# Optimization experiments

Measured on AMD Instinct MI355X. Metric: run time of the kernel, lower is better.

## Reference

```python
import jax, jax.numpy as jnp
import numpy as np

STRIDE = 16.0
PRE = 1000      # rpn_pre_nms_top_n_test
POST = 500      # rpn_post_nms_top_n_test
NMS_TH = 0.7    # rpn_nms_thresh
POOL = 7        # roi align output_size
BBOX_CLIP = float(np.log(1000.0 / 16.0))


def make_anchors(H, W):
    sizes = jnp.array([32., 64., 128., 256.], jnp.float32)
    ratios = jnp.array([0.5, 1.0, 2.0], jnp.float32)
    hr = jnp.sqrt(ratios)
    wr = 1.0 / hr
    ws = (wr[:, None] * sizes[None, :]).reshape(-1)   # [12]
    hs = (hr[:, None] * sizes[None, :]).reshape(-1)
    base = jnp.stack([-ws / 2, -hs / 2, ws / 2, hs / 2], 1)  # [12,4]
    sy = jnp.arange(H, dtype=jnp.float32) * STRIDE
    sx = jnp.arange(W, dtype=jnp.float32) * STRIDE
    gy, gx = jnp.meshgrid(sy, sx, indexing='ij')
    shift = jnp.stack([gx, gy, gx, gy], -1)                  # [H,W,4]
    return (shift[:, :, None, :] + base[None, None]).reshape(-1, 4)  # [H*W*12,4]


def decode(anch, dlt):
    wa = anch[:, 2] - anch[:, 0]
    ha = anch[:, 3] - anch[:, 1]
    cxa = anch[:, 0] + 0.5 * wa
    cya = anch[:, 1] + 0.5 * ha
    dx, dy = dlt[:, 0], dlt[:, 1]
    dw = jnp.minimum(dlt[:, 2], BBOX_CLIP)
    dh = jnp.minimum(dlt[:, 3], BBOX_CLIP)
    cx = dx * wa + cxa
    cy = dy * ha + cya
    w = jnp.exp(dw) * wa
    h = jnp.exp(dh) * ha
    return jnp.stack([cx - 0.5 * w, cy - 0.5 * h, cx + 0.5 * w, cy + 0.5 * h], 1)


def box_iou(a, b):
    area_a = (a[:, 2] - a[:, 0]) * (a[:, 3] - a[:, 1])
    area_b = (b[:, 2] - b[:, 0]) * (b[:, 3] - b[:, 1])
    lt = jnp.maximum(a[:, None, :2], b[None, :, :2])
    rb = jnp.minimum(a[:, None, 2:], b[None, :, 2:])
    wh = jnp.clip(rb - lt, 0.0)
    inter = wh[..., 0] * wh[..., 1]
    return inter / (area_a[:, None] + area_b[None, :] - inter + 1e-6)


def bilinear(feat, ys, xs):
    # feat [C,H,W]; ys/xs [...]; returns [C, ...]
    H, W = feat.shape[1], feat.shape[2]
    ys = jnp.clip(ys, 0.0, H - 1.0)
    xs = jnp.clip(xs, 0.0, W - 1.0)
    y0 = jnp.floor(ys).astype(jnp.int32)
    x0 = jnp.floor(xs).astype(jnp.int32)
    y1 = jnp.minimum(y0 + 1, H - 1)
    x1 = jnp.minimum(x0 + 1, W - 1)
    wy = ys - y0
    wx = xs - x0
    return (feat[:, y0, x0] * (1 - wy) * (1 - wx)
            + feat[:, y0, x1] * (1 - wy) * wx
            + feat[:, y1, x0] * wy * (1 - wx)
            + feat[:, y1, x1] * wy * wx)


def roi_align(feat, boxes):
    # feat [C,H,W], boxes [N,4] in image coords; output_size=7, sampling_ratio=2
    N = boxes.shape[0]
    x1, y1 = boxes[:, 0] / STRIDE, boxes[:, 1] / STRIDE
    x2, y2 = boxes[:, 2] / STRIDE, boxes[:, 3] / STRIDE
    rw = jnp.maximum(x2 - x1, 1.0)
    rh = jnp.maximum(y2 - y1, 1.0)
    bw = rw / POOL
    bh = rh / POOL
    sub = (jnp.arange(2, dtype=jnp.float32) + 0.5) / 2.0  # 2 samples per bin dim
    grid = jnp.arange(POOL, dtype=jnp.float32)
    gy = y1[:, None, None] + (grid[None, :, None] + sub[None, None, :]) * bh[:, None, None]  # [N,7,2]
    gx = x1[:, None, None] + (grid[None, :, None] + sub[None, None, :]) * bw[:, None, None]
    ys = jnp.broadcast_to(gy[:, :, None, :, None], (N, POOL, POOL, 2, 2))
    xs = jnp.broadcast_to(gx[:, None, :, None, :], (N, POOL, POOL, 2, 2))
    v = bilinear(feat, ys, xs)          # [C,N,7,7,2,2]
    v = v.mean(axis=(-1, -2))           # avg over sample points -> [C,N,7,7]
    return v.transpose(1, 0, 2, 3).reshape(N, -1)  # [N, C*49]


def per_image(feat, obj, dlt, anchors, Himg, Wimg):
    sc, idx = jax.lax.top_k(obj, PRE)            # score-sorted (desc) pre-NMS proposals
    boxes = decode(anchors[idx], dlt[idx])
    boxes = jnp.stack([jnp.clip(boxes[:, 0], 0.0, Wimg), jnp.clip(boxes[:, 1], 0.0, Himg),
                       jnp.clip(boxes[:, 2], 0.0, Wimg), jnp.clip(boxes[:, 3], 0.0, Himg)], 1)
    iou = box_iou(boxes, boxes)                  # [PRE,PRE]
    ar = jnp.arange(PRE)

    def body(i, mask):
        cur = mask[i]
        sup = cur & (iou[i] > NMS_TH) & (ar > i)
        return mask & ~sup

    mask = jax.lax.fori_loop(0, PRE, body, jnp.ones((PRE,), bool))
    scm = jnp.where(mask, sc, -jnp.inf)
    _, keep = jax.lax.top_k(scm, POST)           # first POST kept (score order)
    props = boxes[keep]                          # [POST,4]
    return roi_align(feat, props)


def setup_inputs() -> dict:
    key = jax.random.key(0)
    ks = jax.random.split(key, 8)
    s = 0.02
    C, H, W = 960, 20, 40
    return {
        'features': jax.random.normal(ks[0], (2, C, H, W), jnp.float32),
        'rpn_conv_w': jax.random.normal(ks[1], (C, C, 3, 3), jnp.float32) * s,
        'rpn_conv_b': jnp.zeros((C,), jnp.float32),
        'rpn_cls_w': jax.random.normal(ks[2], (12, C), jnp.float32) * s,
        'rpn_cls_b': jnp.zeros((12,), jnp.float32),
        'rpn_reg_w': jax.random.normal(ks[3], (48, C), jnp.float32) * s,
        'rpn_reg_b': jnp.zeros((48,), jnp.float32),
        'fc6_w': jax.random.normal(ks[4], (C * POOL * POOL, 1024), jnp.float32) * s,
        'fc6_b': jnp.zeros((1024,), jnp.float32),
        'fc7_w': jax.random.normal(ks[5], (1024, 1024), jnp.float32) * s,
        'fc7_b': jnp.zeros((1024,), jnp.float32),
        'cls_w': jax.random.normal(ks[6], (1024, 5), jnp.float32) * s,
        'cls_b': jnp.zeros((5,), jnp.float32),
        'bbox_w': jax.random.normal(ks[7], (1024, 20), jnp.float32) * s,
        'bbox_b': jnp.zeros((20,), jnp.float32),
    }


def reference(features, rpn_conv_w, rpn_conv_b, rpn_cls_w, rpn_cls_b,
              rpn_reg_w, rpn_reg_b, fc6_w, fc6_b, fc7_w, fc7_b,
              cls_w, cls_b, bbox_w, bbox_b):
    B, C, H, W = features.shape
    A = 12
    t = jax.lax.conv_general_dilated(features, rpn_conv_w, (1, 1), 'SAME',
                                     dimension_numbers=('NCHW', 'OIHW', 'NCHW'))
    t = jax.nn.relu(t + rpn_conv_b[None, :, None, None])
    obj = (jnp.einsum('bchw,ac->bhwa', t, rpn_cls_w) + rpn_cls_b).reshape(B, -1)  # [B, H*W*A]
    reg = jnp.einsum('bchw,ac->bahw', t, rpn_reg_w) + rpn_reg_b[None, :, None, None]
    reg = reg.reshape(B, A, 4, H, W).transpose(0, 3, 4, 1, 2).reshape(B, -1, 4)   # [B, H*W*A, 4]
    anchors = make_anchors(H, W)
    Himg, Wimg = H * STRIDE, W * STRIDE
    pooled = jax.vmap(lambda f, o, d: per_image(f, o, d, anchors, Himg, Wimg))(
        features, obj, reg)                       # [B, POST, C*49]
    x = jax.nn.relu(pooled @ fc6_w + fc6_b)       # TwoMLPHead fc6
    x = jax.nn.relu(x @ fc7_w + fc7_b)            # TwoMLPHead fc7
    logits = x @ cls_w + cls_b                    # [B, POST, 5]
    breg = x @ bbox_w + bbox_b                    # [B, POST, 20]
    return jnp.concatenate([logits, breg], -1)    # [B, POST, 25]
```

## Files before the change

kernel.cpp:

```cpp
#include <hip/hip_runtime.h>
#include <hip/hip_bf16.h>
#include <cstdint>
#include <cstddef>


typedef __attribute__((ext_vector_type(8))) short short8;
typedef __attribute__((ext_vector_type(4))) float f32x4;

__device__ __forceinline__ void gld_lds16(const void* g, void* l)
{
  __builtin_amdgcn_global_load_lds(
      (const __attribute__((address_space(1))) unsigned int*)g,
      (__attribute__((address_space(3))) unsigned int*)l, 16, 0, 0);
}

__global__ __launch_bounds__(256) void pad_kernel(const float* __restrict__ f,
                                                  float* __restrict__ xp)
{
  int idx = blockIdx.x * 256 + threadIdx.x;
  const int total = 2 * 960 * 22 * 42;
  if (idx >= total) return;
  int xx = idx % 42;
  int r  = idx / 42;
  int yy = r % 22;
  int bc = r / 22;
  float v = 0.f;
  if (yy >= 1 && yy <= 20 && xx >= 1 && xx <= 40)
    v = f[bc * 800 + (yy - 1) * 40 + (xx - 1)];
  xp[idx] = v;
}

__global__ __launch_bounds__(256) void conv_kernel(const float* __restrict__ Wc,
                                                   const float* __restrict__ Xpad,
                                                   const float* __restrict__ bias,
                                                   float* __restrict__ T)
{
  __shared__ float As[16][64];
  __shared__ float Bs[16][64];
  int tid = threadIdx.x;
  int b  = blockIdx.z;
  int p0 = blockIdx.x * 64;
  int m0 = blockIdx.y * 64;
  int ty = tid >> 4, tx = tid & 15;
  int a_m = tid >> 2, a_k4 = (tid & 3) << 2;
  int b_k = tid >> 4, b_p4 = (tid & 15) << 2;
  const float* xb = Xpad + (size_t)b * 960 * 22 * 42;
  float acc[4][4] = {};
  for (int k0 = 0; k0 < 8640; k0 += 16) {
    float4 av = *(const float4*)&Wc[(size_t)(m0 + a_m) * 8640 + k0 + a_k4];
    As[a_k4 + 0][a_m] = av.x; As[a_k4 + 1][a_m] = av.y;
    As[a_k4 + 2][a_m] = av.z; As[a_k4 + 3][a_m] = av.w;
    int k = k0 + b_k;
    int c = k / 9; int tap = k - c * 9;
    int ky = tap / 3; int kx = tap - ky * 3;
    const float* xrow = xb + (c * 22 + ky) * 42 + kx;
#pragma unroll
    for (int u = 0; u < 4; ++u) {
      int p = p0 + b_p4 + u;
      float v = 0.f;
      if (p < 800) { int y = p / 40; int x = p - y * 40; v = xrow[y * 42 + x]; }
      Bs[b_k][b_p4 + u] = v;
    }
    __syncthreads();
#pragma unroll
    for (int kk = 0; kk < 16; ++kk) {
      float a[4], bb[4];
      *(float4*)a  = *(const float4*)&As[kk][ty << 2];
      *(float4*)bb = *(const float4*)&Bs[kk][tx << 2];
#pragma unroll
      for (int i = 0; i < 4; ++i)
#pragma unroll
        for (int j = 0; j < 4; ++j) acc[i][j] += a[i] * bb[j];
    }
    __syncthreads();
  }
#pragma unroll
  for (int i = 0; i < 4; ++i) {
    int o = m0 + (ty << 2) + i;
    float bs = bias[o];
#pragma unroll
    for (int j = 0; j < 4; ++j) {
      int p = p0 + (tx << 2) + j;
      if (p < 800) T[((size_t)b * 960 + o) * 800 + p] = fmaxf(acc[i][j] + bs, 0.f);
    }
  }
}

__global__ __launch_bounds__(256) void rpn_head(const float* __restrict__ t,
                                                const float* __restrict__ cls_w,
                                                const float* __restrict__ cls_b,
                                                const float* __restrict__ reg_w,
                                                const float* __restrict__ reg_b,
                                                float* __restrict__ obj,
                                                float* __restrict__ dlt)
{
  int bp = blockIdx.x;
  int b = bp / 800, p = bp - (bp / 800) * 800;
  __shared__ float tv[960];
  for (int c = threadIdx.x; c < 960; c += 256)
    tv[c] = t[((size_t)b * 960 + c) * 800 + p];
  __syncthreads();
  __shared__ float part[60][4];
  int j = threadIdx.x >> 2, pp = threadIdx.x & 3;
  if (j < 60) {
    const float* wrow = (j < 12) ? &cls_w[j * 960] : &reg_w[(j - 12) * 960];
    float acc = 0.f;
    for (int c = pp; c < 960; c += 4) acc += tv[c] * wrow[c];
    part[j][pp] = acc;
  }
  __syncthreads();
  if (threadIdx.x < 60) {
    int j2 = threadIdx.x;
    float s = part[j2][0] + part[j2][1] + part[j2][2] + part[j2][3];
    if (j2 < 12) {
      obj[(size_t)b * 9600 + p * 12 + j2] = s + cls_b[j2];
    } else {
      int o = j2 - 12;
      dlt[((size_t)b * 9600 + p * 12 + (o >> 2)) * 4 + (o & 3)] = s + reg_b[o];
    }
  }
}

__device__ inline unsigned long long pack_key(float v, int g)
{
  unsigned u = __float_as_uint(v);
  u = (u & 0x80000000u) ? ~u : (u | 0x80000000u);
  return ((unsigned long long)u << 32) | (unsigned)(~g);
}

__global__ __launch_bounds__(512) void sort8k(const float* __restrict__ obj,
                                              unsigned long long* __restrict__ topkeys)
{
  __shared__ unsigned long long keys[8192];
  int b = blockIdx.x >> 1, h = blockIdx.x & 1;
  int tid = threadIdx.x;
  for (int i = tid; i < 8192; i += 512) {
    int g = h * 8192 + i;
    unsigned long long key = 0ULL;
    if (g < 9600) key = pack_key(obj[(size_t)b * 9600 + g], g);
    keys[i] = key;
  }
  __syncthreads();
  for (int k = 2; k <= 8192; k <<= 1)
    for (int j = k >> 1; j > 0; j >>= 1) {
      for (int i = tid; i < 8192; i += 512) {
        int ixj = i ^ j;
        if (ixj > i) {
          bool desc = ((i & k) == 0);
          unsigned long long a = keys[i], c = keys[ixj];
          if ((a < c) == desc) { keys[i] = c; keys[ixj] = a; }
        }
      }
      __syncthreads();
    }
  for (int i = tid; i < 1024; i += 512)
    topkeys[(size_t)blockIdx.x * 1024 + i] = keys[i];
}

__global__ __launch_bounds__(256) void merge2k(const unsigned long long* __restrict__ topkeys,
                                               int* __restrict__ selidx)
{
  __shared__ unsigned long long keys[2048];
  int b = blockIdx.x, tid = threadIdx.x;
  for (int i = tid; i < 2048; i += 256) keys[i] = topkeys[(size_t)b * 2048 + i];
  __syncthreads();
  for (int k = 2; k <= 2048; k <<= 1)
    for (int j = k >> 1; j > 0; j >>= 1) {
      for (int i = tid; i < 2048; i += 256) {
        int ixj = i ^ j;
        if (ixj > i) {
          bool desc = ((i & k) == 0);
          unsigned long long a = keys[i], c = keys[ixj];
          if ((a < c) == desc) { keys[i] = c; keys[ixj] = a; }
        }
      }
      __syncthreads();
    }
  for (int i = tid; i < 1000; i += 256)
    selidx[b * 1000 + i] = (int)(~(unsigned)(keys[i] & 0xffffffffULL));
}

__global__ __launch_bounds__(256) void decode_kernel(const int* __restrict__ selidx,
                                                     const float* __restrict__ dlt,
                                                     float* __restrict__ boxes)
{
#pragma clang fp contract(off)
  int t = blockIdx.x * 256 + threadIdx.x;
  if (t >= 2000) return;
  int b = t / 1000;
  int g = selidx[t];
  int cell = g / 12, a = g - cell * 12;
  int y = cell / 40, x = cell - y * 40;
  int ridx = a >> 2, sidx = a & 3;
  const float sizes_[4]  = {32.f, 64.f, 128.f, 256.f};
  const float ratios_[3] = {0.5f, 1.f, 2.f};
  float size = sizes_[sidx];
  float hr = sqrtf(ratios_[ridx]);
  float wr = 1.f / hr;
  float wsz = wr * size, hsz = hr * size;
  float hw = 0.5f * wsz, hh = 0.5f * hsz;
  float gx = (float)x * 16.f, gy = (float)y * 16.f;
  float a0 = gx - hw, a1 = gy - hh, a2 = gx + hw, a3 = gy + hh;
  float wa = a2 - a0, ha = a3 - a1;
  float cxa = a0 + 0.5f * wa, cya = a1 + 0.5f * ha;
  const float* d = &dlt[(size_t)(b * 9600 + g) * 4];
  float dx = d[0], dy = d[1];
  float dw = fminf(d[2], 4.135166556742356f);
  float dh = fminf(d[3], 4.135166556742356f);
  float cx = dx * wa + cxa;
  float cy = dy * ha + cya;
  float w = expf(dw) * wa;
  float h = expf(dh) * ha;
  float x1 = cx - 0.5f * w, y1 = cy - 0.5f * h;
  float x2 = cx + 0.5f * w, y2 = cy + 0.5f * h;
  x1 = fminf(fmaxf(x1, 0.f), 640.f);
  y1 = fminf(fmaxf(y1, 0.f), 320.f);
  x2 = fminf(fmaxf(x2, 0.f), 640.f);
  y2 = fminf(fmaxf(y2, 0.f), 320.f);
  *(float4*)&boxes[(size_t)t * 4] = make_float4(x1, y1, x2, y2);
}

__global__ __launch_bounds__(256) void iou_kernel(const float* __restrict__ boxes,
                                                  unsigned long long* __restrict__ bitrow)
{
#pragma clang fp contract(off)
  int b = blockIdx.y;
  int i = blockIdx.x * 16 + (threadIdx.x >> 4);
  int w = threadIdx.x & 15;
  __shared__ float4 bx[1000];
  for (int t = threadIdx.x; t < 1000; t += 256)
    bx[t] = *(const float4*)&boxes[(size_t)(b * 1000 + t) * 4];
  __syncthreads();
  if (i >= 1000) return;
  float4 bi = bx[i];
  float area_i = (bi.z - bi.x) * (bi.w - bi.y);
  unsigned long long bits = 0ULL;
  for (int t = 0; t < 64; ++t) {
    int j = w * 64 + t;
    if (j > i && j < 1000) {
      float4 bj = bx[j];
      float xx1 = fmaxf(bi.x, bj.x), yy1 = fmaxf(bi.y, bj.y);
      float xx2 = fminf(bi.z, bj.z), yy2 = fminf(bi.w, bj.w);
      float iw = fmaxf(xx2 - xx1, 0.f), ih = fmaxf(yy2 - yy1, 0.f);
      float inter = iw * ih;
      float area_j = (bj.z - bj.x) * (bj.w - bj.y);
      float iou = inter / (area_i + area_j - inter + 1e-6f);
      if (iou > 0.7f) bits |= 1ULL << t;
    }
  }
  bitrow[(size_t)(b * 1000 + i) * 16 + w] = bits;
}

__device__ inline unsigned long long shfl64(unsigned long long v, int src)
{
  int lo = __shfl((int)(unsigned)(v & 0xffffffffULL), src, 64);
  int hi = __shfl((int)(unsigned)(v >> 32), src, 64);
  return ((unsigned long long)(unsigned)hi << 32) | (unsigned)lo;
}

__global__ __launch_bounds__(64) void nms_scan(const unsigned long long* __restrict__ bitrow,
                                               const float* __restrict__ boxes,
                                               float* __restrict__ props)
{
  int b = blockIdx.x;
  int lane = threadIdx.x;
  unsigned long long alive = 0ULL;
  if (lane < 15) alive = ~0ULL;
  else if (lane == 15) alive = (1ULL << 40) - 1ULL;
  const unsigned long long* rows = bitrow + (size_t)b * 16000;
  for (int i0 = 0; i0 < 1000; i0 += 4) {
    unsigned long long v = rows[i0 * 16 + lane];
#pragma unroll
    for (int s = 0; s < 4; ++s) {
      int i = i0 + s;
      unsigned long long row = shfl64(v, (s << 4) | (lane & 15));
      unsigned long long ow = shfl64(alive, i >> 6);
      if ((ow >> (i & 63)) & 1ULL) alive &= ~row;
    }
  }
  __shared__ unsigned long long am[16];
  __shared__ int keep[500];
  if (lane < 16) am[lane] = alive;
  __syncthreads();
  if (lane == 0) {
    int cnt = 0;
    for (int i = 0; i < 1000 && cnt < 500; ++i)
      if ((am[i >> 6] >> (i & 63)) & 1ULL) keep[cnt++] = i;
    for (int i = 0; i < 1000 && cnt < 500; ++i)
      if (!((am[i >> 6] >> (i & 63)) & 1ULL)) keep[cnt++] = i;
  }
  __syncthreads();
  for (int r = lane; r < 500; r += 64) {
    int g = keep[r];
    *(float4*)&props[(size_t)(b * 500 + r) * 4] =
        *(const float4*)&boxes[(size_t)(b * 1000 + g) * 4];
  }
}

__global__ __launch_bounds__(256) void transpose_feat(const float* __restrict__ f,
                                                      float* __restrict__ ft)
{
  __shared__ float tile[32][33];
  int b = blockIdx.z;
  int c0 = blockIdx.y * 32, p0 = blockIdx.x * 32;
  int tx = threadIdx.x, ty = threadIdx.y;
  for (int r = ty; r < 32; r += 8)
    tile[r][tx] = f[((size_t)b * 960 + c0 + r) * 800 + p0 + tx];
  __syncthreads();
  for (int r = ty; r < 32; r += 8)
    ft[((size_t)b * 800 + p0 + r) * 960 + c0 + tx] = tile[tx][r];
}

__global__ __launch_bounds__(256) void roi_kernel(const float* __restrict__ ft,
                                                  const float* __restrict__ props,
                                                  __hip_bfloat16* __restrict__ pooled)
{
  int q = blockIdx.x;
  int nr = blockIdx.y;
  __hip_bfloat16* outp = pooled + (size_t)nr * 47040 + q * 960;
  if (nr >= 1000) {
    for (int c = threadIdx.x; c < 960; c += 256) outp[c] = __float2bfloat16(0.f);
    return;
  }
  int b = nr / 500;
  int py = q / 7, px = q - py * 7;
  float4 bx = *(const float4*)&props[(size_t)nr * 4];
  float x1 = bx.x / 16.f, y1 = bx.y / 16.f, x2 = bx.z / 16.f, y2 = bx.w / 16.f;
  float rw = fmaxf(x2 - x1, 1.f), rh = fmaxf(y2 - y1, 1.f);
  float bw = rw / 7.f, bh = rh / 7.f;
  int offs[16]; float wts[16];
#pragma unroll
  for (int s = 0; s < 4; ++s) {
    int sy = s >> 1, sx = s & 1;
    float ys = y1 + ((float)py + (sy ? 0.75f : 0.25f)) * bh;
    float xs = x1 + ((float)px + (sx ? 0.75f : 0.25f)) * bw;
    ys = fminf(fmaxf(ys, 0.f), 19.f);
    xs = fminf(fmaxf(xs, 0.f), 39.f);
    int y0 = (int)floorf(ys), x0 = (int)floorf(xs);
    int y1i = y0 + 1 < 19 ? y0 + 1 : 19;
    int x1i = x0 + 1 < 39 ? x0 + 1 : 39;
    float wy = ys - (float)y0, wx = xs - (float)x0;
    int base0 = y0 * 40, base1 = y1i * 40;
    offs[s * 4 + 0] = base0 + x0;  wts[s * 4 + 0] = 0.25f * (1.f - wy) * (1.f - wx);
    offs[s * 4 + 1] = base0 + x1i; wts[s * 4 + 1] = 0.25f * (1.f - wy) * wx;
    offs[s * 4 + 2] = base1 + x0;  wts[s * 4 + 2] = 0.25f * wy * (1.f - wx);
    offs[s * 4 + 3] = base1 + x1i; wts[s * 4 + 3] = 0.25f * wy * wx;
  }
  const float* fb = ft + (size_t)b * 800 * 960;
  for (int c = threadIdx.x; c < 960; c += 256) {
    float acc = 0.f;
#pragma unroll
    for (int s = 0; s < 16; ++s) acc += wts[s] * fb[(size_t)offs[s] * 960 + c];
    outp[c] = __float2bfloat16(acc);
  }
}

__global__ __launch_bounds__(256) void cast_w6(const float* __restrict__ w6,
                                               __hip_bfloat16* __restrict__ WbT)
{
  __shared__ float tile[32][33];
  int c0 = blockIdx.x * 32;
  int n0 = blockIdx.y * 32;
  int q  = blockIdx.z;
  int tx = threadIdx.x & 31, ty = threadIdx.x >> 5;
  for (int rr = ty; rr < 32; rr += 8)
    tile[rr][tx] = w6[((size_t)(c0 + rr) * 49 + q) * 1024 + n0 + tx];
  __syncthreads();
  for (int rr = ty; rr < 32; rr += 8)
    WbT[(size_t)(n0 + rr) * 47040 + q * 960 + c0 + tx] = __float2bfloat16(tile[tx][rr]);
}

__global__ __launch_bounds__(256) void cast_w7(const float* __restrict__ w7,
                                               __hip_bfloat16* __restrict__ WT)
{
  __shared__ float tile[32][33];
  int k0 = blockIdx.x * 32, n0 = blockIdx.y * 32;
  int tx = threadIdx.x & 31, ty = threadIdx.x >> 5;
  for (int rr = ty; rr < 32; rr += 8)
    tile[rr][tx] = w7[(size_t)(k0 + rr) * 1024 + n0 + tx];
  __syncthreads();
  for (int rr = ty; rr < 32; rr += 8)
    WT[(size_t)(n0 + rr) * 1024 + k0 + tx] = __float2bfloat16(tile[tx][rr]);
}

__global__ __launch_bounds__(256, 2) void gemm_bf16(const ushort* __restrict__ A,
                                                    const ushort* __restrict__ BT,
                                                    float* __restrict__ C,
                                                    int Klen, int ksteps, int splitk)
{
  __shared__ __align__(16) ushort As[128 * 32];
  __shared__ __align__(16) ushort Bs[128 * 32];
  int tid = threadIdx.x;
  int wave = tid >> 6, lane = tid & 63;
  int n0 = blockIdx.x * 128, m0 = blockIdx.y * 128;
  int steps_per = (ksteps + splitk - 1) / splitk;
  int s0 = blockIdx.z * steps_per;
  int s1 = min(ksteps, s0 + steps_per);

  const ushort* Ap0 = A  + (size_t)(m0 + wave * 32 + (lane >> 2)) * Klen + ((lane & 3) << 3);
  const ushort* Bp0 = BT + (size_t)(n0 + wave * 32 + (lane >> 2)) * Klen + ((lane & 3) << 3);
  size_t rstep = (size_t)16 * Klen;
  ushort* Al0 = &As[(wave * 32) * 32];
  ushort* Al1 = &As[(wave * 32 + 16) * 32];
  ushort* Bl0 = &Bs[(wave * 32) * 32];
  ushort* Bl1 = &Bs[(wave * 32 + 16) * 32];

  int wm = (wave >> 1) * 64, wn = (wave & 1) * 64;
  int ar = lane & 15, aq = (lane >> 4) << 3;
  f32x4 acc[4][4] = {};

  for (int s = s0; s < s1; ++s) {
    size_t k0 = (size_t)s << 5;
    gld_lds16(Ap0 + k0, Al0);
    gld_lds16(Ap0 + rstep + k0, Al1);
    gld_lds16(Bp0 + k0, Bl0);
    gld_lds16(Bp0 + rstep + k0, Bl1);
    __syncthreads();
    short8 af[4], bfv[4];
#pragma unroll
    for (int mi = 0; mi < 4; ++mi)
      af[mi] = *(const short8*)&As[(wm + mi * 16 + ar) * 32 + aq];
#pragma unroll
    for (int ni = 0; ni < 4; ++ni)
      bfv[ni] = *(const short8*)&Bs[(wn + ni * 16 + ar) * 32 + aq];
#pragma unroll
    for (int mi = 0; mi < 4; ++mi)
#pragma unroll
      for (int ni = 0; ni < 4; ++ni)
        acc[mi][ni] = __builtin_amdgcn_mfma_f32_16x16x32_bf16(af[mi], bfv[ni],
                                                              acc[mi][ni], 0, 0, 0);
    __syncthreads();
  }
  int crow = m0 + wm + ((lane >> 4) << 2);
  int ccol = n0 + wn + (lane & 15);
#pragma unroll
  for (int mi = 0; mi < 4; ++mi)
#pragma unroll
    for (int ni = 0; ni < 4; ++ni) {
      float* cp = &C[(size_t)(crow + mi * 16) * 1024 + ccol + ni * 16];
      f32x4 v = acc[mi][ni];
      atomicAdd(cp,        v.x);
      atomicAdd(cp + 1024, v.y);
      atomicAdd(cp + 2048, v.z);
      atomicAdd(cp + 3072, v.w);
    }
}

__global__ __launch_bounds__(256) void ep_bf16(const float* __restrict__ Cacc,
                                               const float* __restrict__ bias,
                                               __hip_bfloat16* __restrict__ out)
{
  int idx = blockIdx.x * 256 + threadIdx.x;
  out[idx] = __float2bfloat16(fmaxf(Cacc[idx] + bias[idx & 1023], 0.f));
}

__global__ __launch_bounds__(256) void ep_f32(const float* __restrict__ Cacc,
                                              const float* __restrict__ bias,
                                              float* __restrict__ out)
{
  int idx = blockIdx.x * 256 + threadIdx.x;
  out[idx] = fmaxf(Cacc[idx] + bias[idx & 1023], 0.f);
}

__global__ __launch_bounds__(256) void out_head(const float* __restrict__ x2,
                                                const float* __restrict__ cls_w,
                                                const float* __restrict__ cls_b,
                                                const float* __restrict__ bbox_w,
                                                const float* __restrict__ bbox_b,
                                                float* __restrict__ out)
{
  int n = blockIdx.x;
  __shared__ float xv[1024];
  __shared__ float part[25][8];
  for (int k = threadIdx.x; k < 1024; k += 256) xv[k] = x2[(size_t)n * 1024 + k];
  __syncthreads();
  int j = threadIdx.x >> 3, pp = threadIdx.x & 7;
  if (j < 25) {
    float acc = 0.f;
    if (j < 5) {
      for (int k = pp; k < 1024; k += 8) acc += xv[k] * cls_w[k * 5 + j];
    } else {
      int jj = j - 5;
      for (int k = pp; k < 1024; k += 8) acc += xv[k] * bbox_w[k * 20 + jj];
    }
    part[j][pp] = acc;
  }
  __syncthreads();
  if (threadIdx.x < 25) {
    int j2 = threadIdx.x;
    float s = 0.f;
#pragma unroll
    for (int p = 0; p < 8; ++p) s += part[j2][p];
    s += (j2 < 5) ? cls_b[j2] : bbox_b[j2 - 5];
    out[(size_t)n * 25 + j2] = s;
  }
}

extern "C" void kernel_launch(void* const* d_in, const int* in_sizes, int n_in,
                              void* d_out, int out_size, void* d_ws, size_t ws_size,
                              hipStream_t stream)
{
  const float* features  = (const float*)d_in[0];
  const float* conv_w    = (const float*)d_in[1];
  const float* conv_b    = (const float*)d_in[2];
  const float* rpn_cls_w = (const float*)d_in[3];
  const float* rpn_cls_b = (const float*)d_in[4];
  const float* rpn_reg_w = (const float*)d_in[5];
  const float* rpn_reg_b = (const float*)d_in[6];
  const float* fc6_w     = (const float*)d_in[7];
  const float* fc6_b     = (const float*)d_in[8];
  const float* fc7_w     = (const float*)d_in[9];
  const float* fc7_b     = (const float*)d_in[10];
  const float* hd_cls_w  = (const float*)d_in[11];
  const float* hd_cls_b  = (const float*)d_in[12];
  const float* hd_bbox_w = (const float*)d_in[13];
  const float* hd_bbox_b = (const float*)d_in[14];

  char* ws = (char*)d_ws;
  size_t off = 0;
  auto alloc = [&](size_t bytes) -> char* {
    char* p = ws + off;
    off += (bytes + 255) & ~(size_t)255;
    return p;
  };
  float* xpad   = (float*)alloc(2ull * 960 * 22 * 42 * 4);
  float* t      = (float*)alloc(2ull * 960 * 800 * 4);
  float* obj    = (float*)alloc(2ull * 9600 * 4);
  float* dlt    = (float*)alloc(2ull * 9600 * 4 * 4);
  unsigned long long* topkeys = (unsigned long long*)alloc(4ull * 1024 * 8);
  int* selidx   = (int*)alloc(2000ull * 4);
  float* boxes  = (float*)alloc(2ull * 1000 * 4 * 4);
  unsigned long long* bitrow = (unsigned long long*)alloc(2ull * 1000 * 16 * 8);
  float* props  = (float*)alloc(2ull * 500 * 4 * 4);
  float* featT  = (float*)alloc(2ull * 800 * 960 * 4);
  __hip_bfloat16* pooled = (__hip_bfloat16*)alloc(1024ull * 47040 * 2);
  __hip_bfloat16* WbT    = (__hip_bfloat16*)alloc(1024ull * 47040 * 2);
  __hip_bfloat16* fc7T   = (__hip_bfloat16*)alloc(1024ull * 1024 * 2);
  float* Cacc   = (float*)alloc(1024ull * 1024 * 4);
  float* Cacc2  = (float*)alloc(1024ull * 1024 * 4);
  __hip_bfloat16* x1bf = (__hip_bfloat16*)alloc(1024ull * 1024 * 2);
  float* x2buf  = (float*)alloc(1024ull * 1024 * 4);

  hipMemsetAsync(Cacc, 0, 1024ull * 1024 * 4, stream);
  hipMemsetAsync(Cacc2, 0, 1024ull * 1024 * 4, stream);

  pad_kernel<<<(2 * 960 * 22 * 42 + 255) / 256, 256, 0, stream>>>(features, xpad);
  conv_kernel<<<dim3(13, 15, 2), 256, 0, stream>>>(conv_w, xpad, conv_b, t);
  rpn_head<<<1600, 256, 0, stream>>>(t, rpn_cls_w, rpn_cls_b, rpn_reg_w, rpn_reg_b, obj, dlt);
  sort8k<<<4, 512, 0, stream>>>(obj, topkeys);
  merge2k<<<2, 256, 0, stream>>>(topkeys, selidx);
  decode_kernel<<<8, 256, 0, stream>>>(selidx, dlt, boxes);
  iou_kernel<<<dim3(63, 2), 256, 0, stream>>>(boxes, bitrow);
  nms_scan<<<2, 64, 0, stream>>>(bitrow, boxes, props);
  transpose_feat<<<dim3(25, 30, 2), dim3(32, 8), 0, stream>>>(features, featT);
  roi_kernel<<<dim3(49, 1024), 256, 0, stream>>>(featT, props, pooled);
  cast_w6<<<dim3(30, 32, 49), 256, 0, stream>>>(fc6_w, WbT);
  cast_w7<<<dim3(32, 32), 256, 0, stream>>>(fc7_w, fc7T);
  gemm_bf16<<<dim3(8, 8, 8), 256, 0, stream>>>((const ushort*)pooled, (const ushort*)WbT,
                                               Cacc, 47040, 1470, 8);
  ep_bf16<<<4096, 256, 0, stream>>>(Cacc, fc6_b, x1bf);
  gemm_bf16<<<dim3(8, 8, 8), 256, 0, stream>>>((const ushort*)x1bf, (const ushort*)fc7T,
                                               Cacc2, 1024, 32, 8);
  ep_f32<<<4096, 256, 0, stream>>>(Cacc2, fc7_b, x2buf);
  out_head<<<1000, 256, 0, stream>>>(x2buf, hd_cls_w, hd_cls_b, hd_bbox_w, hd_bbox_b,
                                     (float*)d_out);
}
```

Baseline: 2.024 ms.

## Run RPN conv as split-bf16 MFMA GEMM and tile RPN head as GEMM

Replaces the FP32 SIMT 3x3 conv with an im2col GEMM on bf16 MFMA. Each FP32 operand is split into three bf16 parts, and six cross products are accumulated with atomics so precision stays near FP32. The per-pixel RPN head kernel becomes a tiled small GEMM over a padded activation layout. This costs extra preprocessing and memory traffic for the split weights and im2col buffers, plus atomic accumulation, and it reuses the workspace region of the pooled buffer.

```diff
diff --git a/kernel.cpp b/kernel.cpp
--- a/kernel.cpp
+++ b/kernel.cpp
@@ -7,6 +7,10 @@
 typedef __attribute__((ext_vector_type(8))) short short8;
 typedef __attribute__((ext_vector_type(4))) float f32x4;
 
+#define CONV_M 1024
+#define CONV_N 896
+#define CONV_K 8640
+
 __device__ __forceinline__ void gld_lds16(const void* g, void* l)
 {
   __builtin_amdgcn_global_load_lds(
@@ -14,79 +18,165 @@
       (__attribute__((address_space(3))) unsigned int*)l, 16, 0, 0);
 }
 
-__global__ __launch_bounds__(256) void pad_kernel(const float* __restrict__ f,
-                                                  float* __restrict__ xp)
+__device__ __forceinline__ void bf16split3(float v, ushort& o0, ushort& o1, ushort& o2)
+{
+  __hip_bfloat16 h0 = __float2bfloat16(v);
+  float r1 = v - __bfloat162float(h0);
+  __hip_bfloat16 h1 = __float2bfloat16(r1);
+  float r2 = r1 - __bfloat162float(h1);
+  __hip_bfloat16 h2 = __float2bfloat16(r2);
+  o0 = *(ushort*)&h0; o1 = *(ushort*)&h1; o2 = *(ushort*)&h2;
+}
+
+__global__ __launch_bounds__(256) void wsplit(const float* __restrict__ w,
+                                              ushort* __restrict__ Wsp)
 {
   int idx = blockIdx.x * 256 + threadIdx.x;
-  const int total = 2 * 960 * 22 * 42;
-  if (idx >= total) return;
-  int xx = idx % 42;
-  int r  = idx / 42;
-  int yy = r % 22;
-  int bc = r / 22;
+  if (idx >= 960 * 960) return;
+  int c = idx % 960, o = idx / 960;
+  const float* src = w + (size_t)o * 8640 + c * 9;
+  size_t ob = (size_t)o * 8640 + c;
+  const size_t SS = (size_t)CONV_M * CONV_K;
+#pragma unroll
+  for (int tap = 0; tap < 9; ++tap) {
+    ushort b0, b1, b2;
+    bf16split3(src[tap], b0, b1, b2);
+    Wsp[ob + tap * 960]          = b0;
+    Wsp[SS + ob + tap * 960]     = b1;
+    Wsp[2 * SS + ob + tap * 960] = b2;
+  }
+}
+
+__global__ __launch_bounds__(256) void wzero(ushort* __restrict__ Wsp)
+{
+  int idx = blockIdx.x * 256 + threadIdx.x;
+  if (idx >= 3 * 64 * 8640) return;
+  int s = idx / (64 * 8640);
+  int r = idx - s * (64 * 8640);
+  Wsp[(size_t)s * CONV_M * CONV_K + (size_t)960 * CONV_K + r] = 0;
+}
+
+__global__ __launch_bounds__(256) void im2col_split(const float* __restrict__ f,
+                                                    ushort* __restrict__ Xsp)
+{
+  int idx = blockIdx.x * 256 + threadIdx.x;
+  if (idx >= 2 * 896 * 960) return;
+  int c = idx % 960;
+  int r = idx / 960;
+  int p = r % 896;
+  int img = r / 896;
+  const size_t SS = (size_t)2 * CONV_N * CONV_K;
+  size_t ob = ((size_t)img * CONV_N + p) * CONV_K + c;
+  if (p >= 800) {
+#pragma unroll
+    for (int tap = 0; tap < 9; ++tap) {
+      Xsp[ob + tap * 960] = 0;
+      Xsp[SS + ob + tap * 960] = 0;
+      Xsp[2 * SS + ob + tap * 960] = 0;
+    }
+    return;
+  }
+  int y = p / 40, x = p - (p / 40) * 40;
+  const float* fb = f + ((size_t)img * 960 + c) * 800;
+#pragma unroll
+  for (int ky = 0; ky < 3; ++ky)
+#pragma unroll
+    for (int kx = 0; kx < 3; ++kx) {
+      int yy = y + ky - 1, xx = x + kx - 1;
+      float v = (yy >= 0 && yy < 20 && xx >= 0 && xx < 40) ? fb[yy * 40 + xx] : 0.f;
+      ushort b0, b1, b2;
+      bf16split3(v, b0, b1, b2);
+      int tap = ky * 3 + kx;
+      Xsp[ob + tap * 960] = b0;
+      Xsp[SS + ob + tap * 960] = b1;
+      Xsp[2 * SS + ob + tap * 960] = b2;
+    }
+}
+
+__global__ __launch_bounds__(256, 2) void conv_gemm(const ushort* __restrict__ Wsp,
+                                                    const ushort* __restrict__ Xsp,
+                                                    float* __restrict__ Cacc)
+{
+  __shared__ __align__(16) ushort As[128 * 32];
+  __shared__ __align__(16) ushort Bs[128 * 32];
+  const int wi_t[6] = {0, 0, 1, 0, 1, 2};
+  const int xi_t[6] = {0, 1, 0, 2, 1, 0};
+  int z = blockIdx.z;
+  int img = z & 1, prod = z >> 1;
+  const ushort* A  = Wsp + (size_t)wi_t[prod] * CONV_M * CONV_K;
+  const ushort* BT = Xsp + ((size_t)xi_t[prod] * 2 + img) * CONV_N * CONV_K;
+  float* C = Cacc + (size_t)img * CONV_M * CONV_N;
+  const int Klen = CONV_K;
+
+  int tid = threadIdx.x;
+  int wave = tid >> 6, lane = tid & 63;
+  int n0 = blockIdx.x * 128, m0 = blockIdx.y * 128;
+
+  const ushort* Ap0 = A  + (size_t)(m0 + wave * 32 + (lane >> 2)) * Klen + ((lane & 3) << 3);
+  const ushort* Bp0 = BT + (size_t)(n0 + wave * 32 + (lane >> 2)) * Klen + ((lane & 3) << 3);
+  size_t rstep = (size_t)16 * Klen;
+  ushort* Al0 = &As[(wave * 32) * 32];
+  ushort* Al1 = &As[(wave * 32 + 16) * 32];
+  ushort* Bl0 = &Bs[(wave * 32) * 32];
+  ushort* Bl1 = &Bs[(wave * 32 + 16) * 32];
+
+  int wm = (wave >> 1) * 64, wn = (wave & 1) * 64;
+  int ar = lane & 15, aq = (lane >> 4) << 3;
+  f32x4 acc[4][4] = {};
+
+  for (int s = 0; s < CONV_K / 32; ++s) {
+    size_t k0 = (size_t)s << 5;
+    gld_lds16(Ap0 + k0, Al0);
+    gld_lds16(Ap0 + rstep + k0, Al1);
+    gld_lds16(Bp0 + k0, Bl0);
+    gld_lds16(Bp0 + rstep + k0, Bl1);
+    __syncthreads();
+    short8 af[4], bfv[4];
+#pragma unroll
+    for (int mi = 0; mi < 4; ++mi)
+      af[mi] = *(const short8*)&As[(wm + mi * 16 + ar) * 32 + aq];
+#pragma unroll
+    for (int ni = 0; ni < 4; ++ni)
+      bfv[ni] = *(const short8*)&Bs[(wn + ni * 16 + ar) * 32 + aq];
+#pragma unroll
+    for (int mi = 0; mi < 4; ++mi)
+#pragma unroll
+      for (int ni = 0; ni < 4; ++ni)
+        acc[mi][ni] = __builtin_amdgcn_mfma_f32_16x16x32_bf16(af[mi], bfv[ni],
+                                                              acc[mi][ni], 0, 0, 0);
+    __syncthreads();
+  }
+  int crow = m0 + wm + ((lane >> 4) << 2);
+  int ccol = n0 + wn + (lane & 15);
+#pragma unroll
+  for (int mi = 0; mi < 4; ++mi)
+#pragma unroll
+    for (int ni = 0; ni < 4; ++ni) {
+      float* cp = &C[(size_t)(crow + mi * 16) * CONV_N + ccol + ni * 16];
+      f32x4 v = acc[mi][ni];
+      atomicAdd(cp,                v.x);
+      atomicAdd(cp + CONV_N,       v.y);
+      atomicAdd(cp + 2 * CONV_N,   v.z);
+      atomicAdd(cp + 3 * CONV_N,   v.w);
+    }
+}
+
+__global__ __launch_bounds__(256) void conv_ep(const float* __restrict__ Cacc,
+                                               const float* __restrict__ bias,
+                                               float* __restrict__ T)
+{
+  int idx = blockIdx.x * 256 + threadIdx.x;
+  if (idx >= 2 * 960 * 832) return;
+  int p = idx % 832;
+  int r = idx / 832;
+  int o = r % 960;
+  int img = r / 960;
   float v = 0.f;
-  if (yy >= 1 && yy <= 20 && xx >= 1 && xx <= 40)
-    v = f[bc * 800 + (yy - 1) * 40 + (xx - 1)];
-  xp[idx] = v;
-}
-
-__global__ __launch_bounds__(256) void conv_kernel(const float* __restrict__ Wc,
-                                                   const float* __restrict__ Xpad,
-                                                   const float* __restrict__ bias,
-                                                   float* __restrict__ T)
-{
-  __shared__ float As[16][64];
-  __shared__ float Bs[16][64];
-  int tid = threadIdx.x;
-  int b  = blockIdx.z;
-  int p0 = blockIdx.x * 64;
-  int m0 = blockIdx.y * 64;
-  int ty = tid >> 4, tx = tid & 15;
-  int a_m = tid >> 2, a_k4 = (tid & 3) << 2;
-  int b_k = tid >> 4, b_p4 = (tid & 15) << 2;
-  const float* xb = Xpad + (size_t)b * 960 * 22 * 42;
-  float acc[4][4] = {};
-  for (int k0 = 0; k0 < 8640; k0 += 16) {
-    float4 av = *(const float4*)&Wc[(size_t)(m0 + a_m) * 8640 + k0 + a_k4];
-    As[a_k4 + 0][a_m] = av.x; As[a_k4 + 1][a_m] = av.y;
-    As[a_k4 + 2][a_m] = av.z; As[a_k4 + 3][a_m] = av.w;
-    int k = k0 + b_k;
-    int c = k / 9; int tap = k - c * 9;
-    int ky = tap / 3; int kx = tap - ky * 3;
-    const float* xrow = xb + (c * 22 + ky) * 42 + kx;
-#pragma unroll
-    for (int u = 0; u < 4; ++u) {
-      int p = p0 + b_p4 + u;
-      float v = 0.f;
-      if (p < 800) { int y = p / 40; int x = p - y * 40; v = xrow[y * 42 + x]; }
-      Bs[b_k][b_p4 + u] = v;
-    }
-    __syncthreads();
-#pragma unroll
-    for (int kk = 0; kk < 16; ++kk) {
-      float a[4], bb[4];
-      *(float4*)a  = *(const float4*)&As[kk][ty << 2];
-      *(float4*)bb = *(const float4*)&Bs[kk][tx << 2];
-#pragma unroll
-      for (int i = 0; i < 4; ++i)
-#pragma unroll
-        for (int j = 0; j < 4; ++j) acc[i][j] += a[i] * bb[j];
-    }
-    __syncthreads();
-  }
-#pragma unroll
-  for (int i = 0; i < 4; ++i) {
-    int o = m0 + (ty << 2) + i;
-    float bs = bias[o];
-#pragma unroll
-    for (int j = 0; j < 4; ++j) {
-      int p = p0 + (tx << 2) + j;
-      if (p < 800) T[((size_t)b * 960 + o) * 800 + p] = fmaxf(acc[i][j] + bs, 0.f);
-    }
-  }
-}
-
-__global__ __launch_bounds__(256) void rpn_head(const float* __restrict__ t,
+  if (p < 800) v = fmaxf(Cacc[((size_t)img * CONV_M + o) * CONV_N + p] + bias[o], 0.f);
+  T[idx] = v;
+}
+
+__global__ __launch_bounds__(256) void rpn_gemm(const float* __restrict__ T,
                                                 const float* __restrict__ cls_w,
                                                 const float* __restrict__ cls_b,
                                                 const float* __restrict__ reg_w,
@@ -94,29 +184,40 @@
                                                 float* __restrict__ obj,
                                                 float* __restrict__ dlt)
 {
-  int bp = blockIdx.x;
-  int b = bp / 800, p = bp - (bp / 800) * 800;
-  __shared__ float tv[960];
-  for (int c = threadIdx.x; c < 960; c += 256)
-    tv[c] = t[((size_t)b * 960 + c) * 800 + p];
-  __syncthreads();
-  __shared__ float part[60][4];
-  int j = threadIdx.x >> 2, pp = threadIdx.x & 3;
-  if (j < 60) {
-    const float* wrow = (j < 12) ? &cls_w[j * 960] : &reg_w[(j - 12) * 960];
-    float acc = 0.f;
-    for (int c = pp; c < 960; c += 4) acc += tv[c] * wrow[c];
-    part[j][pp] = acc;
-  }
-  __syncthreads();
-  if (threadIdx.x < 60) {
-    int j2 = threadIdx.x;
-    float s = part[j2][0] + part[j2][1] + part[j2][2] + part[j2][3];
-    if (j2 < 12) {
-      obj[(size_t)b * 9600 + p * 12 + j2] = s + cls_b[j2];
-    } else {
-      int o = j2 - 12;
-      dlt[((size_t)b * 9600 + p * 12 + (o >> 2)) * 4 + (o & 3)] = s + reg_b[o];
+  __shared__ float As[16][64];
+  __shared__ float Bs[16][64];
+  int img = blockIdx.y, p0 = blockIdx.x * 64;
+  int tid = threadIdx.x;
+  int aj = tid >> 2, ak = (tid & 3) << 2;
+  int bk = tid >> 4, bp = (tid & 15) << 2;
+  int ty = tid >> 6, tx = tid & 63;
+  float acc[15] = {};
+  const float* Tb = T + (size_t)img * 960 * 832;
+  for (int k0 = 0; k0 < 960; k0 += 16) {
+    if (aj < 60) {
+      const float* wrow = (aj < 12) ? cls_w + aj * 960 : reg_w + (aj - 12) * 960;
+      float4 wv = *(const float4*)&wrow[k0 + ak];
+      As[ak + 0][aj] = wv.x; As[ak + 1][aj] = wv.y;
+      As[ak + 2][aj] = wv.z; As[ak + 3][aj] = wv.w;
+    }
+    *(float4*)&Bs[bk][bp] = *(const float4*)&Tb[(size_t)(k0 + bk) * 832 + p0 + bp];
+    __syncthreads();
+#pragma unroll
+    for (int kk = 0; kk < 16; ++kk) {
+      float bv = Bs[kk][tx];
+#pragma unroll
+      for (int jj = 0; jj < 15; ++jj) acc[jj] += As[kk][jj * 4 + ty] * bv;
+    }
+    __syncthreads();
+  }
+  int p = p0 + tx;
+  if (p < 800) {
+#pragma unroll
+    for (int jj = 0; jj < 15; ++jj) {
+      int j = jj * 4 + ty;
+      float val = acc[jj] + ((j < 12) ? cls_b[j] : reg_b[j - 12]);
+      if (j < 12) obj[(size_t)img * 9600 + p * 12 + j] = val;
+      else        dlt[(size_t)img * 38400 + p * 48 + (j - 12)] = val;
     }
   }
 }
@@ -523,8 +624,7 @@
     off += (bytes + 255) & ~(size_t)255;
     return p;
   };
-  float* xpad   = (float*)alloc(2ull * 960 * 22 * 42 * 4);
-  float* t      = (float*)alloc(2ull * 960 * 800 * 4);
+  float* T      = (float*)alloc(2ull * 960 * 832 * 4);
   float* obj    = (float*)alloc(2ull * 9600 * 4);
   float* dlt    = (float*)alloc(2ull * 9600 * 4 * 4);
   unsigned long long* topkeys = (unsigned long long*)alloc(4ull * 1024 * 8);
@@ -533,25 +633,37 @@
   unsigned long long* bitrow = (unsigned long long*)alloc(2ull * 1000 * 16 * 8);
   float* props  = (float*)alloc(2ull * 500 * 4 * 4);
   float* featT  = (float*)alloc(2ull * 800 * 960 * 4);
-  __hip_bfloat16* pooled = (__hip_bfloat16*)alloc(1024ull * 47040 * 2);
-  __hip_bfloat16* WbT    = (__hip_bfloat16*)alloc(1024ull * 47040 * 2);
-  __hip_bfloat16* fc7T   = (__hip_bfloat16*)alloc(1024ull * 1024 * 2);
+  __hip_bfloat16* fc7T = (__hip_bfloat16*)alloc(1024ull * 1024 * 2);
   float* Cacc   = (float*)alloc(1024ull * 1024 * 4);
   float* Cacc2  = (float*)alloc(1024ull * 1024 * 4);
   __hip_bfloat16* x1bf = (__hip_bfloat16*)alloc(1024ull * 1024 * 2);
   float* x2buf  = (float*)alloc(1024ull * 1024 * 4);
 
-  hipMemsetAsync(Cacc, 0, 1024ull * 1024 * 4, stream);
+  size_t uoff = off;
+  ushort* Xsp  = (ushort*)(ws + uoff);
+  ushort* Wsp  = Xsp + 3ull * 2 * CONV_N * CONV_K;
+  float*  CaccC = (float*)(Wsp + 3ull * CONV_M * CONV_K);
+  __hip_bfloat16* pooled = (__hip_bfloat16*)(ws + uoff);
+  __hip_bfloat16* WbT    = pooled + 1024ull * 47040;
+
+  hipMemsetAsync(CaccC, 0, 2ull * CONV_M * CONV_N * 4, stream);
+  hipMemsetAsync(Cacc,  0, 1024ull * 1024 * 4, stream);
   hipMemsetAsync(Cacc2, 0, 1024ull * 1024 * 4, stream);
 
-  pad_kernel<<<(2 * 960 * 22 * 42 + 255) / 256, 256, 0, stream>>>(features, xpad);
-  conv_kernel<<<dim3(13, 15, 2), 256, 0, stream>>>(conv_w, xpad, conv_b, t);
-  rpn_head<<<1600, 256, 0, stream>>>(t, rpn_cls_w, rpn_cls_b, rpn_reg_w, rpn_reg_b, obj, dlt);
+  wsplit<<<(960 * 960 + 255) / 256, 256, 0, stream>>>(conv_w, Wsp);
+  wzero<<<(3 * 64 * 8640 + 255) / 256, 256, 0, stream>>>(Wsp);
+  im2col_split<<<(2 * 896 * 960 + 255) / 256, 256, 0, stream>>>(features, Xsp);
+  conv_gemm<<<dim3(7, 8, 12), 256, 0, stream>>>(Wsp, Xsp, CaccC);
+  conv_ep<<<(2 * 960 * 832 + 255) / 256, 256, 0, stream>>>(CaccC, conv_b, T);
+
+  rpn_gemm<<<dim3(13, 2), 256, 0, stream>>>(T, rpn_cls_w, rpn_cls_b, rpn_reg_w, rpn_reg_b,
+                                            obj, dlt);
   sort8k<<<4, 512, 0, stream>>>(obj, topkeys);
   merge2k<<<2, 256, 0, stream>>>(topkeys, selidx);
   decode_kernel<<<8, 256, 0, stream>>>(selidx, dlt, boxes);
   iou_kernel<<<dim3(63, 2), 256, 0, stream>>>(boxes, bitrow);
   nms_scan<<<2, 64, 0, stream>>>(bitrow, boxes, props);
+
   transpose_feat<<<dim3(25, 30, 2), dim3(32, 8), 0, stream>>>(features, featT);
   roi_kernel<<<dim3(49, 1024), 256, 0, stream>>>(featT, props, pooled);
   cast_w6<<<dim3(30, 32, 49), 256, 0, stream>>>(fc6_w, WbT);
```

Measured after the change: 1.687 ms. 1.2x faster.
